# Kernel tuning notes

Measured on AMD Instinct MI355X. Metric: run time of the kernel, lower is better.

The kernel has to match this reference:

```python
import jax, jax.numpy as jnp
import numpy as np

B, N, H, NH, DEPTH = 4, 128, 512, 8, 4
HD = H // NH
TN = B * N
MH = int(H * 4.0)
EHD = 64
SCALE = HD ** -0.5

def _ln(x):
    m = jnp.mean(x, axis=-1, keepdims=True)
    v = jnp.mean(jnp.square(x - m), axis=-1, keepdims=True)
    return (x - m) * jax.lax.rsqrt(v + 1e-6)

def _gelu(x):
    return jax.nn.gelu(x, approximate=True)

def setup_inputs():
    rng = np.random.RandomState(0)
    topo_np = (rng.rand(B, N, N) < 0.15).astype(np.float32)
    sym = (topo_np + topo_np.transpose(0, 2, 1)) > 0
    b, i, j = np.nonzero(sym)  # same lexicographic order as torch nonzero
    edge_index = np.stack([i + b * N, j + b * N]).astype(np.int32)
    ks = jax.random.split(jax.random.key(0), 16)
    def w(k, shape, fan_in):
        return jax.random.normal(k, shape, jnp.float32) / np.float32(np.sqrt(fan_in))
    z = lambda *s: jnp.zeros(s, jnp.float32)
    return {
        "topo": jnp.asarray(topo_np),
        "weight": jax.random.normal(ks[0], (B, N), jnp.float32),
        "edge_index": jnp.asarray(edge_index),
        "w_topo": w(ks[1], (N, H), N), "b_topo": z(H),
        "w_w": w(ks[2], (1, H), 1), "b_w": z(H),
        "n_emb": 0.02 * jax.random.normal(ks[3], (N, H), jnp.float32),
        "wq": w(ks[4], (DEPTH, H, H), H), "bq": z(DEPTH, H),
        "wk": w(ks[5], (DEPTH, H, H), H), "bk": z(DEPTH, H),
        "wv": w(ks[6], (DEPTH, H, H), H), "bv": z(DEPTH, H),
        "wo": w(ks[7], (DEPTH, H, H), H), "bo": z(DEPTH, H),
        "w1": w(ks[8], (DEPTH, H, MH), H), "b1": z(DEPTH, MH),
        "w2": w(ks[9], (DEPTH, MH, H), MH), "b2": z(DEPTH, H),
        "ew1": w(ks[10], (3 * H, EHD), 3 * H), "eb1": z(EHD),
        "ew2": w(ks[11], (EHD, EHD), EHD), "eb2": z(EHD),
        "ew3": w(ks[12], (EHD, 1), EHD), "eb3": z(1),
    }

def _forward(topo, weight, edge_index, w_topo, b_topo, w_w, b_w, n_emb,
             wq, bq, wk, bk, wv, bv, wo, bo, w1, b1, w2, b2,
             ew1, eb1, ew2, eb2, ew3, eb3):
    src, dst = edge_index[0], edge_index[1]
    tsym = topo + jnp.swapaxes(topo, 1, 2)                      # (B,N,N)
    t = jnp.einsum('bnm,mh->bnh', tsym, w_topo) + b_topo        # topo_emb
    l = weight[..., None] * w_w[0] + b_w                        # weight_emb: Linear(1,H)
    x = (t + l + n_emb[None]).reshape(TN, H)
    for d in range(DEPTH):
        h = _ln(x)
        Q = (h @ wq[d] + bq[d]).reshape(TN, NH, HD)
        K = (h @ wk[d] + bk[d]).reshape(TN, NH, HD)
        V = (h @ wv[d] + bv[d]).reshape(TN, NH, HD)
        s = jnp.einsum('ehd,ehd->eh', Q[dst], K[src]) * SCALE   # (E,NH) per-edge QK dot
        m = jnp.maximum(jax.ops.segment_max(s, dst, num_segments=TN), -1e9)
        e = jnp.exp(s - m[dst])
        zs = jax.ops.segment_sum(e, dst, num_segments=TN)
        aw = e / (zs[dst] + 1e-12)                              # scatter_softmax
        msg = aw[..., None] * V[src]                            # (E,NH,HD)
        agg = jax.ops.segment_sum(msg, dst, num_segments=TN).reshape(TN, H)
        x = agg @ wo[d] + bo[d] + x
        h = _ln(x)
        x = _gelu(h @ w1[d] + b1[d]) @ w2[d] + b2[d] + x
    xb = x.reshape(B, N, H)
    xi = jnp.broadcast_to(xb[:, :, None, :], (B, N, N, H))
    xj = jnp.broadcast_to(xb[:, None, :, :], (B, N, N, H))
    f = jnp.concatenate([xi, xj, xi * xj], axis=-1)             # (B,N,N,3H)
    g = _gelu(f @ ew1 + eb1)
    g = _gelu(g @ ew2 + eb2)
    p = jax.nn.sigmoid((g @ ew3 + eb3)[..., 0])
    p = 0.5 * (p + jnp.swapaxes(p, 1, 2))
    p = p * (1.0 - jnp.eye(N, dtype=p.dtype))                   # zero diagonal
    p = p * (tsym > 0).astype(p.dtype)                          # mask to existing edges
    return p

def reference(topo, weight, edge_index, w_topo, b_topo, w_w, b_w, n_emb,
              wq, bq, wk, bk, wv, bv, wo, bo, w1, b1, w2, b2,
              ew1, eb1, ew2, eb2, ew3, eb3):
    return _forward(topo, weight, edge_index, w_topo, b_topo, w_w, b_w, n_emb,
                    wq, bq, wk, bk, wv, bv, wo, bo, w1, b1, w2, b2,
                    ew1, eb1, ew2, eb2, ew3, eb3)
```

## Files before the change

kernel.cpp:

```cpp
#include <hip/hip_runtime.h>
#include <hip/hip_bf16.h>
#include <math.h>

typedef __attribute__((ext_vector_type(8))) _Float16 f16x8;
typedef __attribute__((ext_vector_type(8))) short short8;
typedef __attribute__((ext_vector_type(4))) float f32x4;
typedef unsigned short u16;

__device__ __forceinline__ float gelu_f(float x) {
    float x3 = x * x * x;
    return 0.5f * x * (1.0f + tanhf(0.7978845608028654f * (x + 0.044715f * x3)));
}
__device__ __forceinline__ u16 f2h(float v) {
    _Float16 h = (_Float16)v;
    return *(u16*)&h;
}

__global__ __launch_bounds__(256) void x0row_k(const float* __restrict__ topo,
                                               const float* __restrict__ weight,
                                               const float* __restrict__ w_topo,
                                               const float* __restrict__ b_topo,
                                               const float* __restrict__ w_w,
                                               const float* __restrict__ b_w,
                                               const float* __restrict__ n_emb,
                                               float* __restrict__ tsym,
                                               float* __restrict__ x,
                                               u16* __restrict__ h16) {
    int bn = blockIdx.x;
    int b = bn >> 7, n = bn & 127;
    int tid = threadIdx.x;
    __shared__ float tsr[128];
    __shared__ float red[256];
    if (tid < 128) {
        float v = topo[bn * 128 + tid] + topo[(b << 14) + (tid << 7) + n];
        tsr[tid] = v;
        tsym[bn * 128 + tid] = v;
    }
    __syncthreads();
    int c0 = tid, c1 = tid + 256;
    float acc0 = 0.f, acc1 = 0.f;
#pragma unroll 4
    for (int m = 0; m < 128; ++m) {
        float t = tsr[m];
        acc0 += t * w_topo[m * 512 + c0];
        acc1 += t * w_topo[m * 512 + c1];
    }
    float wgt = weight[bn];
    float v0 = acc0 + b_topo[c0] + wgt * w_w[c0] + b_w[c0] + n_emb[n * 512 + c0];
    float v1 = acc1 + b_topo[c1] + wgt * w_w[c1] + b_w[c1] + n_emb[n * 512 + c1];
    x[bn * 512 + c0] = v0;
    x[bn * 512 + c1] = v1;
    red[tid] = v0 + v1;
    __syncthreads();
    for (int off = 128; off > 0; off >>= 1) { if (tid < off) red[tid] += red[tid + off]; __syncthreads(); }
    float mean = red[0] * (1.0f / 512.0f);
    __syncthreads();
    float d0 = v0 - mean, d1 = v1 - mean;
    red[tid] = d0 * d0 + d1 * d1;
    __syncthreads();
    for (int off = 128; off > 0; off >>= 1) { if (tid < off) red[tid] += red[tid + off]; __syncthreads(); }
    float rs = rsqrtf(red[0] * (1.0f / 512.0f) + 1e-6f);
    h16[bn * 512 + c0] = f2h(d0 * rs);
    h16[bn * 512 + c1] = f2h(d1 * rs);
}

__global__ __launch_bounds__(256) void prep_k(
    const float* __restrict__ wq, const float* __restrict__ wk, const float* __restrict__ wv,
    const float* __restrict__ wo, const float* __restrict__ w1, const float* __restrict__ w2,
    const float* __restrict__ ew1,
    u16* __restrict__ qkvt, u16* __restrict__ wot,
    u16* __restrict__ w1t, u16* __restrict__ w2t,
    u16* __restrict__ eabt, u16* __restrict__ ect) {
    __shared__ u16 Hs[64][68];
    int bid = blockIdx.x;
    int region, tr, KK;
    u16* dh;
    if (bid < 768)       { region = 0; tr = bid;        KK = 512;  dh = qkvt; }
    else if (bid < 1024) { region = 1; tr = bid - 768;  KK = 512;  dh = wot; }
    else if (bid < 2048) { region = 2; tr = bid - 1024; KK = 512;  dh = w1t; }
    else if (bid < 3072) { region = 3; tr = bid - 2048; KK = 2048; dh = w2t; }
    else if (bid < 3088) { region = 4; tr = bid - 3072; KK = 512;  dh = eabt; }
    else                 { region = 5; tr = bid - 3088; KK = 512;  dh = ect; }
    int ktiles = KK >> 6;
    int tn = tr / ktiles, tk = tr % ktiles;
    int k0 = tk * 64, n0g = tn * 64;
    int tid = threadIdx.x;
#pragma unroll
    for (int p = 0; p < 4; ++p) {
        int kk = p * 16 + (tid >> 4);
        int nn = (tid & 15) * 4;
        int kg = k0 + kk, ng = n0g + nn;
        const float* src;
        if (region == 0) {
            int d = ng / 1536; int nr = ng - d * 1536; int sel = nr >> 9; int nc = nr & 511;
            const float* w = sel == 0 ? wq : (sel == 1 ? wk : wv);
            src = w + ((size_t)(d * 512 + kg)) * 512 + nc;
        } else if (region == 1) {
            int d = ng >> 9; int nc = ng & 511;
            src = wo + ((size_t)(d * 512 + kg)) * 512 + nc;
        } else if (region == 2) {
            int d = ng >> 11; int nc = ng & 2047;
            src = w1 + ((size_t)(d * 512 + kg)) * 2048 + nc;
        } else if (region == 3) {
            int d = ng >> 9; int nc = ng & 511;
            src = w2 + ((size_t)(d * 2048 + kg)) * 512 + nc;
        } else if (region == 4) {
            src = (ng < 64) ? (ew1 + (size_t)kg * 64 + ng) : (ew1 + (size_t)(512 + kg) * 64 + (ng - 64));
        } else {
            src = ew1 + (size_t)(1024 + kg) * 64 + ng;
        }
        float4 v = *(const float4*)src;
        *(ushort4*)&Hs[kk][nn] = make_ushort4(f2h(v.x), f2h(v.y), f2h(v.z), f2h(v.w));
    }
    __syncthreads();
#pragma unroll
    for (int p = 0; p < 2; ++p) {
        int chunk = p * 256 + tid;
        int nl = chunk >> 3;
        int k8 = (chunk & 7) * 8;
        ushort4 ha, hb;
        ha.x = Hs[k8 + 0][nl]; ha.y = Hs[k8 + 1][nl]; ha.z = Hs[k8 + 2][nl]; ha.w = Hs[k8 + 3][nl];
        hb.x = Hs[k8 + 4][nl]; hb.y = Hs[k8 + 5][nl]; hb.z = Hs[k8 + 6][nl]; hb.w = Hs[k8 + 7][nl];
        size_t dst = (size_t)(n0g + nl) * KK + k0 + k8;
        *(ushort4*)(dh + dst) = ha; *(ushort4*)(dh + dst + 4) = hb;
    }
}

template <int KC, bool PARTIAL, bool GELU, bool RES, bool OUTF, bool OUTS, bool EBIAS>
__global__ __launch_bounds__(256) void gemm2(
    const u16* __restrict__ A16, const u16* __restrict__ W16,
    const float* __restrict__ bias, const float* __restrict__ Rres,
    float* __restrict__ C, u16* __restrict__ C16,
    float* __restrict__ part, int lda, int N) {
    __shared__ u16 sbuf[2][2][64][32];
    const int tid = threadIdx.x;
    const int l = tid & 63;
    const int w = tid >> 6;
    const int bn0 = blockIdx.x * 64;
    const int bm0 = blockIdx.y * 64;
    const int z = blockIdx.z;

    const u16* gp[2];
#pragma unroll
    for (int i = 0; i < 2; ++i) {
        int o = (i * 4 + w) * 1024 + l * 16;
        int mat = o >> 12;
        int r = (o >> 6) & 63;
        int slot = (o >> 4) & 3;
        int lslot = slot ^ ((r >> 1) & 3);
        int kel = lslot * 8;
        const u16* basep = mat == 0 ? (A16 + (size_t)(bm0 + r) * lda)
                                    : (W16 + (size_t)(bn0 + r) * lda);
        gp[i] = basep + kel + z * KC;
    }

    f32x4 acc[2][2] = {};
    constexpr int S = KC / 32;

    auto stage = [&](int buf, int ko) {
#pragma unroll
        for (int i = 0; i < 2; ++i) {
            __builtin_amdgcn_global_load_lds(
                (const __attribute__((address_space(1))) void*)(gp[i] + ko),
                (__attribute__((address_space(3))) void*)((char*)&sbuf[buf][0][0][0] + (i * 4 + w) * 1024),
                16, 0, 0);
        }
    };
    auto compute = [&](int buf) {
        f16x8 a[2], b[2];
        int l15 = l & 15, lsl = l >> 4;
        int rA0 = (w & 1) * 32 + l15;
        int rB0 = (w >> 1) * 32 + l15;
#pragma unroll
        for (int f = 0; f < 2; ++f) {
            int rA = rA0 + f * 16;
            int rB = rB0 + f * 16;
            a[f] = *(const f16x8*)&sbuf[buf][0][rA][(lsl ^ ((rA >> 1) & 3)) * 8];
            b[f] = *(const f16x8*)&sbuf[buf][1][rB][(lsl ^ ((rB >> 1) & 3)) * 8];
        }
#pragma unroll
        for (int fm = 0; fm < 2; ++fm)
#pragma unroll
            for (int fn = 0; fn < 2; ++fn)
                acc[fm][fn] = __builtin_amdgcn_mfma_f32_16x16x32_f16(a[fm], b[fn], acc[fm][fn], 0, 0, 0);
    };

    stage(0, 0);
    __syncthreads();
#pragma unroll
    for (int s = 0; s < S; ++s) {
        if (s + 1 < S) stage((s + 1) & 1, (s + 1) * 32);
        compute(s & 1);
        __syncthreads();
    }

    int rb = bm0 + (w & 1) * 32 + ((l >> 4)) * 4;
    int cb = bn0 + (w >> 1) * 32 + (l & 15);
#pragma unroll
    for (int fm = 0; fm < 2; ++fm)
#pragma unroll
        for (int fn = 0; fn < 2; ++fn) {
            int col = cb + fn * 16;
            float bv;
            if (PARTIAL) bv = 0.f;
            else if (EBIAS) bv = col < 64 ? bias[col] : 0.f;
            else bv = bias[col];
#pragma unroll
            for (int r = 0; r < 4; ++r) {
                int row = rb + fm * 16 + r;
                float v = acc[fm][fn][r] + bv;
                if (PARTIAL) {
                    part[(size_t)z * 512 * N + (size_t)row * N + col] = v;
                } else {
                    if (GELU) v = gelu_f(v);
                    if (RES) v += Rres[(size_t)row * N + col];
                    if (OUTF) C[(size_t)row * N + col] = v;
                    if (OUTS) C16[(size_t)row * N + col] = f2h(v);
                }
            }
        }
}

template <int NZ, bool DOLN, bool DOSPLITX>
__global__ __launch_bounds__(256) void redln_k(const float* __restrict__ part,
                                               const float* __restrict__ bias,
                                               float* __restrict__ x,
                                               u16* __restrict__ h16) {
    int row = blockIdx.x;
    int tid = threadIdx.x;
    int c0 = tid, c1 = tid + 256;
    float v0 = bias[c0], v1 = bias[c1];
#pragma unroll
    for (int z = 0; z < NZ; ++z) {
        v0 += part[(size_t)z * 262144 + row * 512 + c0];
        v1 += part[(size_t)z * 262144 + row * 512 + c1];
    }
    v0 += x[row * 512 + c0];
    v1 += x[row * 512 + c1];
    x[row * 512 + c0] = v0;
    x[row * 512 + c1] = v1;
    if (DOSPLITX) {
        h16[row * 512 + c0] = f2h(v0);
        h16[row * 512 + c1] = f2h(v1);
    }
    if (DOLN) {
        __shared__ float red[256];
        red[tid] = v0 + v1;
        __syncthreads();
        for (int off = 128; off > 0; off >>= 1) { if (tid < off) red[tid] += red[tid + off]; __syncthreads(); }
        float mean = red[0] * (1.0f / 512.0f);
        __syncthreads();
        float d0 = v0 - mean, d1 = v1 - mean;
        red[tid] = d0 * d0 + d1 * d1;
        __syncthreads();
        for (int off = 128; off > 0; off >>= 1) { if (tid < off) red[tid] += red[tid + off]; __syncthreads(); }
        float rs = rsqrtf(red[0] * (1.0f / 512.0f) + 1e-6f);
        h16[row * 512 + c0] = f2h(d0 * rs);
        h16[row * 512 + c1] = f2h(d1 * rs);
    }
}

__global__ __launch_bounds__(256) void attn_k(const float* __restrict__ pw,
                                              const float* __restrict__ bq,
                                              const float* __restrict__ bk,
                                              const float* __restrict__ bv,
                                              const float* __restrict__ tsym,
                                              u16* __restrict__ agg16) {
    int tt = blockIdx.x, hh = blockIdx.y, b = blockIdx.z;
    __shared__ __align__(16) float Ks[128 * 68];
    __shared__ __align__(16) float Vt[64 * 132];
    __shared__ __align__(16) float Ss[16 * 132];
    __shared__ __align__(16) float Qs[16][68];
    int tid = threadIdx.x;
    {
        int j = tid >> 1, c0 = (tid & 1) * 32;
        const float* kr0 = pw + (size_t)(b * 128 + j) * 1536 + 512 + hh * 64 + c0;
        const float* kr1 = kr0 + 786432;
        const float* bkp = bk + hh * 64 + c0;
        const float* bvp = bv + hh * 64 + c0;
#pragma unroll
        for (int c = 0; c < 32; c += 4) {
            float4 k0v = *(const float4*)(kr0 + c);
            float4 k1v = *(const float4*)(kr1 + c);
            float4 v0v = *(const float4*)(kr0 + 512 + c);
            float4 v1v = *(const float4*)(kr1 + 512 + c);
            float4 bkv = *(const float4*)(bkp + c);
            float4 bvv = *(const float4*)(bvp + c);
            Ks[j * 68 + c0 + c + 0] = k0v.x + k1v.x + bkv.x;
            Ks[j * 68 + c0 + c + 1] = k0v.y + k1v.y + bkv.y;
            Ks[j * 68 + c0 + c + 2] = k0v.z + k1v.z + bkv.z;
            Ks[j * 68 + c0 + c + 3] = k0v.w + k1v.w + bkv.w;
            Vt[(c0 + c + 0) * 132 + j] = v0v.x + v1v.x + bvv.x;
            Vt[(c0 + c + 1) * 132 + j] = v0v.y + v1v.y + bvv.y;
            Vt[(c0 + c + 2) * 132 + j] = v0v.z + v1v.z + bvv.z;
            Vt[(c0 + c + 3) * 132 + j] = v0v.w + v1v.w + bvv.w;
        }
    }
    {
        int rid = tid >> 4, c4 = (tid & 15) * 4;
        int grow = b * 128 + tt * 16 + rid;
        const float* q0 = pw + (size_t)grow * 1536 + hh * 64 + c4;
        float4 a = *(const float4*)q0;
        float4 a1 = *(const float4*)(q0 + 786432);
        float4 bb = *(const float4*)(bq + hh * 64 + c4);
        Qs[rid][c4 + 0] = a.x + a1.x + bb.x;
        Qs[rid][c4 + 1] = a.y + a1.y + bb.y;
        Qs[rid][c4 + 2] = a.z + a1.z + bb.z;
        Qs[rid][c4 + 3] = a.w + a1.w + bb.w;
    }
    __syncthreads();
    {
        int j = tid & 127, th = tid >> 7;
        float acc[8] = {0.f, 0.f, 0.f, 0.f, 0.f, 0.f, 0.f, 0.f};
        for (int d0 = 0; d0 < 64; d0 += 4) {
            float4 kv = *(const float4*)&Ks[j * 68 + d0];
#pragma unroll
            for (int r = 0; r < 8; ++r) {
                float4 qv = *(const float4*)&Qs[th * 8 + r][d0];
                acc[r] += qv.x * kv.x + qv.y * kv.y + qv.z * kv.z + qv.w * kv.w;
            }
        }
        const float* tsr = tsym + ((size_t)b << 14) + (size_t)(tt * 16 + th * 8) * 128 + j;
#pragma unroll
        for (int r = 0; r < 8; ++r) {
            int t = th * 8 + r;
            float sv = (tsr[r * 128] > 0.f) ? acc[r] * 0.125f : -INFINITY;
            Ss[t * 132 + j] = sv;
        }
    }
    __syncthreads();
    {
        int row = tid >> 4, l16 = tid & 15;
        float v[8]; float m = -INFINITY;
#pragma unroll
        for (int c = 0; c < 8; ++c) { v[c] = Ss[row * 132 + l16 + c * 16]; m = fmaxf(m, v[c]); }
#pragma unroll
        for (int off = 8; off; off >>= 1) m = fmaxf(m, __shfl_xor(m, off));
        float ssum = 0.f;
#pragma unroll
        for (int c = 0; c < 8; ++c) {
            float e = (v[c] == -INFINITY) ? 0.f : __expf(v[c] - m);
            v[c] = e; ssum += e;
        }
#pragma unroll
        for (int off = 8; off; off >>= 1) ssum += __shfl_xor(ssum, off);
        float inv = 1.0f / (ssum + 1e-12f);
#pragma unroll
        for (int c = 0; c < 8; ++c) Ss[row * 132 + l16 + c * 16] = v[c] * inv;
    }
    __syncthreads();
    {
        int d = tid & 63, tq = tid >> 6;
        float a0 = 0.f, a1 = 0.f, a2 = 0.f, a3 = 0.f;
        for (int j0 = 0; j0 < 128; j0 += 4) {
            float4 vv = *(const float4*)&Vt[d * 132 + j0];
            float4 s0 = *(const float4*)&Ss[(tq * 4 + 0) * 132 + j0];
            float4 s1 = *(const float4*)&Ss[(tq * 4 + 1) * 132 + j0];
            float4 s2 = *(const float4*)&Ss[(tq * 4 + 2) * 132 + j0];
            float4 s3 = *(const float4*)&Ss[(tq * 4 + 3) * 132 + j0];
            a0 += s0.x * vv.x + s0.y * vv.y + s0.z * vv.z + s0.w * vv.w;
            a1 += s1.x * vv.x + s1.y * vv.y + s1.z * vv.z + s1.w * vv.w;
            a2 += s2.x * vv.x + s2.y * vv.y + s2.z * vv.z + s2.w * vv.w;
            a3 += s3.x * vv.x + s3.y * vv.y + s3.z * vv.z + s3.w * vv.w;
        }
        float accv[4] = {a0, a1, a2, a3};
        int growbase = b * 128 + tt * 16;
#pragma unroll
        for (int i = 0; i < 4; ++i) {
            int t = tq * 4 + i;
            agg16[(size_t)(growbase + t) * 512 + hh * 64 + d] = f2h(accv[i]);
        }
    }
}

__global__ __launch_bounds__(256) void redae_k(const float* __restrict__ part,
                                               const float* __restrict__ eb1,
                                               float* __restrict__ aebe) {
    int idx = blockIdx.x * 256 + threadIdx.x;
    int col = idx & 127;
    float v = col < 64 ? eb1[col] : 0.0f;
#pragma unroll
    for (int z = 0; z < 4; ++z) v += part[(size_t)z * 65536 + idx];
    aebe[idx] = v;
}

__global__ __launch_bounds__(256) void cross_k(const float* __restrict__ x,
                                               const u16* __restrict__ ect,
                                               float* __restrict__ C3) {
    int i = blockIdx.x, b = blockIdx.y;
    __shared__ float xis[512];
    __shared__ u16 As[2][128][32];
    int tid = threadIdx.x;
    {
        const float* xip = x + (size_t)(b * 128 + i) * 512;
        xis[tid] = xip[tid];
        xis[tid + 256] = xip[tid + 256];
    }
    int r = tid >> 1, half = tid & 1, koff = half * 16;
    const float* xr = x + (size_t)(b * 128 + r) * 512 + koff;
    int sw_r = (r >> 1) & 3;
    int lane = tid & 63, w = tid >> 6;
    int m0 = (w & 1) * 64, n0 = (w >> 1) * 32;
    int l15 = lane & 15, lsl = lane >> 4, kf = lsl * 8;
    const u16* pB0 = ect + (size_t)(n0 + l15) * 512 + kf;
    const u16* pB1 = ect + (size_t)(n0 + 16 + l15) * 512 + kf;
    f32x4 acc[4][2] = {};

    auto stageA = [&](int buf, int kbase) {
        float4 v0 = *(const float4*)(xr + kbase);
        float4 v1 = *(const float4*)(xr + kbase + 4);
        float4 v2 = *(const float4*)(xr + kbase + 8);
        float4 v3 = *(const float4*)(xr + kbase + 12);
        float xv[16] = {v0.x, v0.y, v0.z, v0.w, v1.x, v1.y, v1.z, v1.w,
                        v2.x, v2.y, v2.z, v2.w, v3.x, v3.y, v3.z, v3.w};
        short8 h0, h1;
#pragma unroll
        for (int q = 0; q < 8; ++q)
            h0[q] = (short)f2h(xv[q] * xis[kbase + koff + q]);
#pragma unroll
        for (int q = 0; q < 8; ++q)
            h1[q] = (short)f2h(xv[8 + q] * xis[kbase + koff + 8 + q]);
        *(short8*)&As[buf][r][((2 * half + 0) ^ sw_r) * 8] = h0;
        *(short8*)&As[buf][r][((2 * half + 1) ^ sw_r) * 8] = h1;
    };
    auto computeC = [&](int buf, int kbase) {
        f16x8 b0 = *(const f16x8*)(pB0 + kbase);
        f16x8 b1 = *(const f16x8*)(pB1 + kbase);
#pragma unroll
        for (int mf = 0; mf < 4; ++mf) {
            int rA = m0 + mf * 16 + l15;
            f16x8 ah = *(const f16x8*)&As[buf][rA][(lsl ^ ((rA >> 1) & 3)) * 8];
            acc[mf][0] = __builtin_amdgcn_mfma_f32_16x16x32_f16(ah, b0, acc[mf][0], 0, 0, 0);
            acc[mf][1] = __builtin_amdgcn_mfma_f32_16x16x32_f16(ah, b1, acc[mf][1], 0, 0, 0);
        }
    };

    __syncthreads();
    stageA(0, 0);
    __syncthreads();
    for (int s = 0; s < 16; ++s) {
        if (s < 15) stageA((s + 1) & 1, (s + 1) * 32);
        computeC(s & 1, s * 32);
        __syncthreads();
    }

    float* outp = C3 + (size_t)(b * 128 + i) * 128 * 64;
#pragma unroll
    for (int mf = 0; mf < 4; ++mf)
#pragma unroll
        for (int nf = 0; nf < 2; ++nf)
#pragma unroll
            for (int q = 0; q < 4; ++q)
                outp[(size_t)(m0 + mf * 16 + lsl * 4 + q) * 64 + (n0 + nf * 16 + l15)] = acc[mf][nf][q];
}

__global__ __launch_bounds__(256) void efin_k(const int* __restrict__ ei, int E,
                                              const float* __restrict__ C3,
                                              const float* __restrict__ aebe,
                                              const float* __restrict__ ew2, const float* __restrict__ eb2,
                                              const float* __restrict__ ew3, const float* __restrict__ eb3,
                                              float* __restrict__ P) {
    __shared__ float G1[32][66];
    __shared__ float G2[32][66];
    __shared__ int s_src[32], s_dst[32];
    int tid = threadIdx.x;
    int e0 = blockIdx.x * 32;
    if (tid < 32) {
        int e = e0 + tid;
        s_src[tid] = e < E ? ei[e] : 0;
        s_dst[tid] = e < E ? ei[E + e] : 0;
    }
    __syncthreads();
    {
        int e = tid >> 3, c8 = (tid & 7) * 8;
        int s = s_src[e], d = s_dst[e];
        int bB = s >> 7, i2 = s & 127, j2 = d & 127;
        const float* c3 = C3 + ((size_t)(bB * 128 + i2) * 128 + j2) * 64 + c8;
        const float* ap = aebe + (size_t)s * 128 + c8;
        const float* bp = aebe + (size_t)d * 128 + 64 + c8;
#pragma unroll
        for (int q = 0; q < 8; ++q)
            G1[e][c8 + q] = gelu_f(c3[q] + ap[q] + bp[q]);
    }
    __syncthreads();
    {
        int col = tid & 63, eq = tid >> 6;
        float acc[8];
#pragma unroll
        for (int i = 0; i < 8; ++i) acc[i] = eb2[col];
        for (int m = 0; m < 64; ++m) {
            float wv = ew2[m * 64 + col];
#pragma unroll
            for (int i = 0; i < 8; ++i) acc[i] += G1[eq * 8 + i][m] * wv;
        }
#pragma unroll
        for (int i = 0; i < 8; ++i) G2[eq * 8 + i][col] = gelu_f(acc[i]);
    }
    __syncthreads();
    {
        int el2 = tid >> 3, c8 = (tid & 7) * 8;
        float p = 0.f;
#pragma unroll
        for (int i = 0; i < 8; ++i) p += G2[el2][c8 + i] * ew3[c8 + i];
        p += __shfl_xor(p, 1); p += __shfl_xor(p, 2); p += __shfl_xor(p, 4);
        if ((tid & 7) == 0 && e0 + el2 < E) {
            float logit = p + eb3[0];
            int s = s_src[el2], d2 = s_dst[el2];
            int bB = s >> 7, i2 = s & 127, j2 = d2 & 127;
            P[(bB << 14) + (i2 << 7) + j2] = 1.0f / (1.0f + expf(-logit));
        }
    }
}

__global__ __launch_bounds__(256) void final_k(const float* __restrict__ tsym,
                                               const float* __restrict__ P,
                                               float* __restrict__ out) {
    int idx = blockIdx.x * 256 + threadIdx.x;
    int b = idx >> 14, i = (idx >> 7) & 127, j = idx & 127;
    float o = 0.0f;
    if (i != j && tsym[idx] > 0.0f)
        o = 0.5f * (P[idx] + P[(b << 14) + (j << 7) + i]);
    out[idx] = o;
}

extern "C" void kernel_launch(void* const* d_in, const int* in_sizes, int n_in,
                              void* d_out, int out_size, void* d_ws, size_t ws_size,
                              hipStream_t stream) {
    const float* topo   = (const float*)d_in[0];
    const float* weight = (const float*)d_in[1];
    const int*   ei     = (const int*)d_in[2];
    const float* w_topo = (const float*)d_in[3];
    const float* b_topo = (const float*)d_in[4];
    const float* w_w    = (const float*)d_in[5];
    const float* b_w    = (const float*)d_in[6];
    const float* n_emb  = (const float*)d_in[7];
    const float* wq = (const float*)d_in[8];  const float* bq = (const float*)d_in[9];
    const float* wk = (const float*)d_in[10]; const float* bk = (const float*)d_in[11];
    const float* wv = (const float*)d_in[12]; const float* bv = (const float*)d_in[13];
    const float* wo = (const float*)d_in[14]; const float* bo = (const float*)d_in[15];
    const float* w1 = (const float*)d_in[16]; const float* b1 = (const float*)d_in[17];
    const float* w2 = (const float*)d_in[18]; const float* b2 = (const float*)d_in[19];
    const float* ew1 = (const float*)d_in[20]; const float* eb1 = (const float*)d_in[21];
    const float* ew2 = (const float*)d_in[22]; const float* eb2 = (const float*)d_in[23];
    const float* ew3 = (const float*)d_in[24]; const float* eb3 = (const float*)d_in[25];
    const int E = in_sizes[2] / 2;

    char* base = (char*)d_ws;
    size_t off = 0;
    auto alloc = [&](size_t bytes) { char* p = base + off; off += (bytes + 255) & ~(size_t)255; return p; };
    u16* qkvt = (u16*)alloc(3145728 * 2);
    u16* wot  = (u16*)alloc(1048576 * 2);
    u16* w1t  = (u16*)alloc(4194304 * 2);
    u16* w2t  = (u16*)alloc(4194304 * 2);
    u16* eabt = (u16*)alloc(65536 * 2);
    u16* ect  = (u16*)alloc(32768 * 2);
    u16* h16   = (u16*)alloc(262144 * 2);
    u16* agg16 = (u16*)alloc(262144 * 2);
    u16* mid16 = (u16*)alloc(1048576 * 2);
    u16* x16   = (u16*)alloc(262144 * 2);
    float* tsym  = (float*)alloc(65536 * 4);
    float* x     = (float*)alloc(262144 * 4);
    float* aebe  = (float*)alloc(65536 * 4);
    float* P     = (float*)alloc(65536 * 4);
    float* pw    = (float*)alloc(1572864 * 4);
    float* C3    = (float*)alloc((size_t)16777216 * 4);

    prep_k<<<3096, 256, 0, stream>>>(wq, wk, wv, wo, w1, w2, ew1,
                                     qkvt, wot, w1t, w2t, eabt, ect);
    x0row_k<<<512, 256, 0, stream>>>(topo, weight, w_topo, b_topo, w_w, b_w, n_emb,
                                     tsym, x, h16);

    for (int d = 0; d < 4; ++d) {
        gemm2<256, true, false, false, false, false, false><<<dim3(24, 8, 2), 256, 0, stream>>>(
            h16, qkvt + (size_t)d * 1536 * 512,
            nullptr, nullptr, nullptr, nullptr, pw, 512, 1536);
        attn_k<<<dim3(8, 8, 4), 256, 0, stream>>>(pw, bq + d * 512, bk + d * 512, bv + d * 512,
                                                  tsym, agg16);
        gemm2<128, true, false, false, false, false, false><<<dim3(8, 8, 4), 256, 0, stream>>>(
            agg16, wot + (size_t)d * 512 * 512,
            nullptr, nullptr, nullptr, nullptr, pw, 512, 512);
        redln_k<4, true, false><<<512, 256, 0, stream>>>(pw, bo + d * 512, x, h16);
        gemm2<512, false, true, false, false, true, false><<<dim3(32, 8, 1), 256, 0, stream>>>(
            h16, w1t + (size_t)d * 2048 * 512,
            b1 + d * 2048, nullptr, nullptr, mid16, nullptr, 512, 2048);
        gemm2<512, true, false, false, false, false, false><<<dim3(8, 8, 4), 256, 0, stream>>>(
            mid16, w2t + (size_t)d * 512 * 2048,
            nullptr, nullptr, nullptr, nullptr, pw, 2048, 512);
        if (d < 3) {
            redln_k<4, true, false><<<512, 256, 0, stream>>>(pw, b2 + d * 512, x, h16);
        } else {
            redln_k<4, false, true><<<512, 256, 0, stream>>>(pw, b2 + d * 512, x, x16);
        }
    }

    gemm2<128, true, false, false, false, false, false><<<dim3(2, 8, 4), 256, 0, stream>>>(
        x16, eabt, nullptr, nullptr, nullptr, nullptr, pw, 512, 128);
    redae_k<<<256, 256, 0, stream>>>(pw, eb1, aebe);
    cross_k<<<dim3(128, 4), 256, 0, stream>>>(x, ect, C3);
    efin_k<<<(E + 31) / 32, 256, 0, stream>>>(ei, E, C3, aebe, ew2, eb2, ew3, eb3, P);
    final_k<<<256, 256, 0, stream>>>(tsym, P, (float*)d_out);
}
```

Before: 292.3 us.

## Increase split-K across transformer GEMMs and split FFN1 with separate GELU reduce

Doubles the split-K factor on the QKV, output-projection and FFN2 GEMMs so each launch has more blocks, and changes the reductions and the attention loader to sum 4 or 8 partial slices. FFN1 is no longer a single fused GEMM with bias and GELU. It now runs as a 2-way split-K GEMM writing float partials, followed by a new reduction kernel that adds the bias, applies GELU and writes fp16. This aims to fill more of the GPU's compute units on these small GEMMs, at the cost of more partial-sum memory traffic, a larger workspace and an extra kernel launch per layer.

```diff
diff --git a/kernel.cpp b/kernel.cpp
--- a/kernel.cpp
+++ b/kernel.cpp
@@ -260,6 +260,20 @@
     }
 }
 
+__global__ __launch_bounds__(256) void redg_k(const float* __restrict__ part,
+                                              const float* __restrict__ bias,
+                                              u16* __restrict__ mid16) {
+    int row = blockIdx.x;
+    int tid = threadIdx.x;
+#pragma unroll
+    for (int u = 0; u < 8; ++u) {
+        int col = tid + u * 256;
+        float v = bias[col] + part[(size_t)row * 2048 + col]
+                + part[(size_t)1048576 + row * 2048 + col];
+        mid16[(size_t)row * 2048 + col] = f2h(gelu_f(v));
+    }
+}
+
 __global__ __launch_bounds__(256) void attn_k(const float* __restrict__ pw,
                                               const float* __restrict__ bq,
                                               const float* __restrict__ bk,
@@ -275,38 +289,42 @@
     {
         int j = tid >> 1, c0 = (tid & 1) * 32;
         const float* kr0 = pw + (size_t)(b * 128 + j) * 1536 + 512 + hh * 64 + c0;
-        const float* kr1 = kr0 + 786432;
         const float* bkp = bk + hh * 64 + c0;
         const float* bvp = bv + hh * 64 + c0;
 #pragma unroll
         for (int c = 0; c < 32; c += 4) {
-            float4 k0v = *(const float4*)(kr0 + c);
-            float4 k1v = *(const float4*)(kr1 + c);
-            float4 v0v = *(const float4*)(kr0 + 512 + c);
-            float4 v1v = *(const float4*)(kr1 + 512 + c);
             float4 bkv = *(const float4*)(bkp + c);
             float4 bvv = *(const float4*)(bvp + c);
-            Ks[j * 68 + c0 + c + 0] = k0v.x + k1v.x + bkv.x;
-            Ks[j * 68 + c0 + c + 1] = k0v.y + k1v.y + bkv.y;
-            Ks[j * 68 + c0 + c + 2] = k0v.z + k1v.z + bkv.z;
-            Ks[j * 68 + c0 + c + 3] = k0v.w + k1v.w + bkv.w;
-            Vt[(c0 + c + 0) * 132 + j] = v0v.x + v1v.x + bvv.x;
-            Vt[(c0 + c + 1) * 132 + j] = v0v.y + v1v.y + bvv.y;
-            Vt[(c0 + c + 2) * 132 + j] = v0v.z + v1v.z + bvv.z;
-            Vt[(c0 + c + 3) * 132 + j] = v0v.w + v1v.w + bvv.w;
+            float k0 = bkv.x, k1 = bkv.y, k2 = bkv.z, k3 = bkv.w;
+            float v0 = bvv.x, v1 = bvv.y, v2 = bvv.z, v3 = bvv.w;
+#pragma unroll
+            for (int z = 0; z < 4; ++z) {
+                float4 kv = *(const float4*)(kr0 + (size_t)z * 786432 + c);
+                float4 vv = *(const float4*)(kr0 + (size_t)z * 786432 + 512 + c);
+                k0 += kv.x; k1 += kv.y; k2 += kv.z; k3 += kv.w;
+                v0 += vv.x; v1 += vv.y; v2 += vv.z; v3 += vv.w;
+            }
+            Ks[j * 68 + c0 + c + 0] = k0; Ks[j * 68 + c0 + c + 1] = k1;
+            Ks[j * 68 + c0 + c + 2] = k2; Ks[j * 68 + c0 + c + 3] = k3;
+            Vt[(c0 + c + 0) * 132 + j] = v0; Vt[(c0 + c + 1) * 132 + j] = v1;
+            Vt[(c0 + c + 2) * 132 + j] = v2; Vt[(c0 + c + 3) * 132 + j] = v3;
         }
     }
     {
         int rid = tid >> 4, c4 = (tid & 15) * 4;
         int grow = b * 128 + tt * 16 + rid;
         const float* q0 = pw + (size_t)grow * 1536 + hh * 64 + c4;
-        float4 a = *(const float4*)q0;
-        float4 a1 = *(const float4*)(q0 + 786432);
         float4 bb = *(const float4*)(bq + hh * 64 + c4);
-        Qs[rid][c4 + 0] = a.x + a1.x + bb.x;
-        Qs[rid][c4 + 1] = a.y + a1.y + bb.y;
-        Qs[rid][c4 + 2] = a.z + a1.z + bb.z;
-        Qs[rid][c4 + 3] = a.w + a1.w + bb.w;
+        float q0v = bb.x, q1v = bb.y, q2v = bb.z, q3v = bb.w;
+#pragma unroll
+        for (int z = 0; z < 4; ++z) {
+            float4 a = *(const float4*)(q0 + (size_t)z * 786432);
+            q0v += a.x; q1v += a.y; q2v += a.z; q3v += a.w;
+        }
+        Qs[rid][c4 + 0] = q0v;
+        Qs[rid][c4 + 1] = q1v;
+        Qs[rid][c4 + 2] = q2v;
+        Qs[rid][c4 + 3] = q3v;
     }
     __syncthreads();
     {
@@ -562,7 +580,7 @@
     float* x     = (float*)alloc(262144 * 4);
     float* aebe  = (float*)alloc(65536 * 4);
     float* P     = (float*)alloc(65536 * 4);
-    float* pw    = (float*)alloc(1572864 * 4);
+    float* pw    = (float*)alloc(3145728 * 4);
     float* C3    = (float*)alloc((size_t)16777216 * 4);
 
     prep_k<<<3096, 256, 0, stream>>>(wq, wk, wv, wo, w1, w2, ew1,
@@ -571,25 +589,26 @@
                                      tsym, x, h16);
 
     for (int d = 0; d < 4; ++d) {
-        gemm2<256, true, false, false, false, false, false><<<dim3(24, 8, 2), 256, 0, stream>>>(
+        gemm2<128, true, false, false, false, false, false><<<dim3(24, 8, 4), 256, 0, stream>>>(
             h16, qkvt + (size_t)d * 1536 * 512,
             nullptr, nullptr, nullptr, nullptr, pw, 512, 1536);
         attn_k<<<dim3(8, 8, 4), 256, 0, stream>>>(pw, bq + d * 512, bk + d * 512, bv + d * 512,
                                                   tsym, agg16);
-        gemm2<128, true, false, false, false, false, false><<<dim3(8, 8, 4), 256, 0, stream>>>(
+        gemm2<64, true, false, false, false, false, false><<<dim3(8, 8, 8), 256, 0, stream>>>(
             agg16, wot + (size_t)d * 512 * 512,
             nullptr, nullptr, nullptr, nullptr, pw, 512, 512);
-        redln_k<4, true, false><<<512, 256, 0, stream>>>(pw, bo + d * 512, x, h16);
-        gemm2<512, false, true, false, false, true, false><<<dim3(32, 8, 1), 256, 0, stream>>>(
+        redln_k<8, true, false><<<512, 256, 0, stream>>>(pw, bo + d * 512, x, h16);
+        gemm2<256, true, false, false, false, false, false><<<dim3(32, 8, 2), 256, 0, stream>>>(
             h16, w1t + (size_t)d * 2048 * 512,
-            b1 + d * 2048, nullptr, nullptr, mid16, nullptr, 512, 2048);
-        gemm2<512, true, false, false, false, false, false><<<dim3(8, 8, 4), 256, 0, stream>>>(
+            nullptr, nullptr, nullptr, nullptr, pw, 512, 2048);
+        redg_k<<<512, 256, 0, stream>>>(pw, b1 + d * 2048, mid16);
+        gemm2<256, true, false, false, false, false, false><<<dim3(8, 8, 8), 256, 0, stream>>>(
             mid16, w2t + (size_t)d * 512 * 2048,
             nullptr, nullptr, nullptr, nullptr, pw, 2048, 512);
         if (d < 3) {
-            redln_k<4, true, false><<<512, 256, 0, stream>>>(pw, b2 + d * 512, x, h16);
+            redln_k<8, true, false><<<512, 256, 0, stream>>>(pw, b2 + d * 512, x, h16);
         } else {
-            redln_k<4, false, true><<<512, 256, 0, stream>>>(pw, b2 + d * 512, x, x16);
+            redln_k<8, false, true><<<512, 256, 0, stream>>>(pw, b2 + d * 512, x, x16);
         }
     }
 
```

Result: slower. 447.7 us (+53.2%).
